# Performance work log

Measured on AMD Instinct MI355X. Metric: run time of the kernel, lower is better.

Reference implementation:

```python
import jax, jax.numpy as jnp
import numpy as np

B, N, E = 8192, 54, 144
F_NODE, F_EDGE, H, OUT = 18, 5, 48, 80
L = 3  # gnn_layers
LN_EPS = 1e-5


def mish(x):
    return x * jnp.tanh(jax.nn.softplus(x))


def setup_inputs() -> dict:
    key = jax.random.key(0)
    ks = jax.random.split(key, 24)
    s = 0.05
    inp = {
        "node_features": jax.random.normal(ks[0], (B, N, F_NODE), jnp.float32),
        "edge_features": jax.random.normal(ks[1], (B, E, F_EDGE), jnp.float32),
        # input projections
        "w_node": jax.random.normal(ks[2], (F_NODE, H), jnp.float32) * s,
        "b_node": jnp.zeros((H,), jnp.float32),
        "w_edge": jax.random.normal(ks[3], (F_EDGE, H), jnp.float32) * s,
        "b_edge": jnp.zeros((H,), jnp.float32),
        # stacked per-layer params (leading dim = L)
        "msg_w1": jax.random.normal(ks[4], (L, 3 * H, H), jnp.float32) * s,
        "msg_b1": jnp.zeros((L, H), jnp.float32),
        "msg_w2": jax.random.normal(ks[5], (L, H, H), jnp.float32) * s,
        "msg_b2": jnp.zeros((L, H), jnp.float32),
        "upd_w1": jax.random.normal(ks[6], (L, 2 * H, H), jnp.float32) * s,
        "upd_b1": jnp.zeros((L, H), jnp.float32),
        "upd_w2": jax.random.normal(ks[7], (L, H, H), jnp.float32) * s,
        "upd_b2": jnp.zeros((L, H), jnp.float32),
        "ln_g": jnp.ones((L, H), jnp.float32),
        "ln_b": jnp.zeros((L, H), jnp.float32),
        # output projection
        "w_out1": jax.random.normal(ks[8], (2 * H, OUT), jnp.float32) * s,
        "b_out1": jnp.zeros((OUT,), jnp.float32),
        "w_out2": jax.random.normal(ks[9], (OUT, OUT), jnp.float32) * s,
        "b_out2": jnp.zeros((OUT,), jnp.float32),
        "edge_index": jax.random.randint(ks[10], (2, E), 0, N, jnp.int64)
        if jax.config.jax_enable_x64 else jax.random.randint(ks[10], (2, E), 0, N, jnp.int32),
    }
    return inp


def reference(node_features, edge_features, w_node, b_node, w_edge, b_edge,
              msg_w1, msg_b1, msg_w2, msg_b2,
              upd_w1, upd_b1, upd_w2, upd_b2, ln_g, ln_b,
              w_out1, b_out1, w_out2, b_out2, edge_index):
    Bv, Nv, _ = node_features.shape
    Ev = edge_features.shape[1]
    h = mish(node_features @ w_node + b_node)            # [B,N,H]
    e = edge_features @ w_edge + b_edge                  # [B,E,H]
    h_flat = h.reshape(Bv * Nv, H)
    e_flat = e.reshape(Bv * Ev, H)
    offsets = jnp.arange(Bv, dtype=edge_index.dtype) * Nv
    src = (edge_index[0][None, :] + offsets[:, None]).reshape(-1)  # [B*E]
    dst = (edge_index[1][None, :] + offsets[:, None]).reshape(-1)
    for l in range(L):
        m = jnp.concatenate([h_flat[src], h_flat[dst], e_flat], axis=-1)  # [B*E,3H]
        m = mish(m @ msg_w1[l] + msg_b1[l])
        m = mish(m @ msg_w2[l] + msg_b2[l])
        agg = jax.ops.segment_sum(m, dst, num_segments=Bv * Nv)  # scatter-add
        u = jnp.concatenate([h_flat, agg], axis=-1)              # [B*N,2H]
        u = mish(u @ upd_w1[l] + upd_b1[l])
        u = u @ upd_w2[l] + upd_b2[l]
        x = h_flat + u
        mu = jnp.mean(x, axis=-1, keepdims=True)
        var = jnp.mean((x - mu) ** 2, axis=-1, keepdims=True)
        h_flat = (x - mu) * jax.lax.rsqrt(var + LN_EPS) * ln_g[l] + ln_b[l]
    node_emb = h_flat.reshape(Bv, Nv, H)
    mean_pool = node_emb.mean(axis=1)
    max_pool = node_emb.max(axis=1)
    pooled = jnp.concatenate([mean_pool, max_pool], axis=-1)     # [B,2H]
    board_emb = mish(pooled @ w_out1 + b_out1) @ w_out2 + b_out2  # [B,OUT]
    return board_emb, node_emb
```

## Files before the change

kernel.cpp:

```cpp
#include <hip/hip_runtime.h>

#define NGR 8192
#define NN 54
#define NE 144
#define FN 18
#define FE 5
#define HD 48
#define NOUT 80
#define NL 3
#define HS 56
#define MS 72
#define TS 152
#define NFRAG 102

typedef short v8s __attribute__((ext_vector_type(8)));
typedef float v4f __attribute__((ext_vector_type(4)));

#define MFMA(a, b, c) __builtin_amdgcn_mfma_f32_16x16x32_bf16((a), (b), (c), 0, 0, 0)

static __device__ __forceinline__ float mish_f(float x) {
  float t = __expf(x);
  float s = 1.0f + t;
  float s2 = s * s;
  float r = (s2 - 1.0f) * __builtin_amdgcn_rcpf(s2 + 1.0f);
  return (x > 20.0f) ? x : x * r;
}
static __device__ __forceinline__ short f2b(float x) {
  union { float f; unsigned u; } v; v.f = x;
  unsigned r = v.u + 0x7FFFu + ((v.u >> 16) & 1u);
  return (short)(r >> 16);
}
static __device__ __forceinline__ float b2f(short s) {
  union { unsigned u; float f; } v; v.u = ((unsigned)(unsigned short)s) << 16;
  return v.f;
}
static __device__ __forceinline__ unsigned pk2(float a, float b) {
  return (unsigned)(unsigned short)f2b(a) | ((unsigned)(unsigned short)f2b(b) << 16);
}

__global__ void gnn_setup(const float* __restrict__ w_node,
                          const float* __restrict__ w_edge,
                          const float* __restrict__ b_edge,
                          const float* __restrict__ msg_w1,
                          const float* __restrict__ msg_b1,
                          const float* __restrict__ msg_w2,
                          const float* __restrict__ upd_w1,
                          const float* __restrict__ upd_w2,
                          float* __restrict__ mb1, short* __restrict__ frags) {
  const int t = threadIdx.x;
  if (blockIdx.x == 0) {
    for (int idx = t; idx < NL * HD; idx += 256) {
      int l = idx / HD, c = idx % HD;
      float s = msg_b1[l * HD + c];
      for (int k = 0; k < HD; ++k)
        s += b_edge[k] * msg_w1[(l * 144 + 96 + k) * HD + c];
      mb1[idx] = s;
    }
  }
  for (int eid = blockIdx.x * 256 + t; eid < NFRAG * 512; eid += gridDim.x * 256) {
    int f = eid >> 9, r = eid & 511;
    int lane = r >> 3, j = r & 7;
    int kk = ((lane >> 4) << 3) + j;
    int colq = lane & 15;
    float val = 0.f;
    if (f < 3) {
      int c = f * 16 + colq;
      if (kk < FN) val = w_node[kk * HD + c];
    } else {
      int g = f - 3, l = g / 33, o = g % 33;
      if (o < 9) {
        int ks = o / 3, ct = o % 3, c = ct * 16 + colq, k = ks * 32 + kk;
        val = msg_w1[(l * 144 + k) * HD + c];
      } else if (o < 12) {
        int ct = o - 9, c = ct * 16 + colq;
        if (kk < FE) {
          float s = 0.f;
          for (int k2 = 0; k2 < HD; ++k2)
            s += w_edge[kk * HD + k2] * msg_w1[(l * 144 + 96 + k2) * HD + c];
          val = s;
        }
      } else if (o < 18) {
        int oo = o - 12, ks = oo / 3, ct = oo % 3, c = ct * 16 + colq, k = ks * 32 + kk;
        if (k < HD) val = msg_w2[(l * HD + k) * HD + c];
      } else if (o < 27) {
        int oo = o - 18, ks = oo / 3, ct = oo % 3, c = ct * 16 + colq, k = ks * 32 + kk;
        val = upd_w1[(l * 96 + k) * HD + c];
      } else {
        int oo = o - 27, ks = oo / 3, ct = oo % 3, c = ct * 16 + colq, k = ks * 32 + kk;
        if (k < HD) val = upd_w2[(l * HD + k) * HD + c];
      }
    }
    frags[eid] = f2b(val);
  }
}

__global__ __launch_bounds__(256, 4) void gnn_main(
    const float* __restrict__ nf, const float* __restrict__ efx,
    const float* __restrict__ b_node,
    const float* __restrict__ msg_b2,
    const float* __restrict__ upd_b1, const float* __restrict__ upd_b2,
    const float* __restrict__ ln_g, const float* __restrict__ ln_b,
    const float* __restrict__ w_out1, const float* __restrict__ b_out1,
    const float* __restrict__ w_out2, const float* __restrict__ b_out2,
    const int* __restrict__ edge_index,
    const float* __restrict__ mb1, const short* __restrict__ frags,
    float* __restrict__ out)
{
  __shared__ __align__(16) short h_s[NN][HS];
  __shared__ __align__(16) short agg_s[NN][HS];
  __shared__ __align__(16) short m_s[80][MS];
  __shared__ __align__(16) short m_t[48 * TS + 8];
  __shared__ int dst_s[NE];
  __shared__ float psum[96], pmax[96], pooled[96], o1[NOUT];

  const int b = blockIdx.x;
  const int t = threadIdx.x;
  const int lane = t & 63;
  const int w = t >> 6;
  const int lx = lane & 15;
  const int lg = lane >> 4;
  const int koff = lg << 3;
  const int lg4 = lg << 2;

#define LD8(f) (*(const v8s*)(frags + ((size_t)(f) << 9) + (lane << 3)))

  if (t < NE) dst_s[t] = edge_index[NE + t];
  for (int idx = t; idx < 64 * 32; idx += 256) {
    int r = idx >> 5, c = idx & 31;
    m_s[r][c] = (r < NN && c < FN) ? f2b(nf[(size_t)b * (NN * FN) + r * FN + c]) : (short)0;
  }
  for (int idx = t; idx < 80 * 16; idx += 256)
    m_s[idx >> 4][48 + (idx & 15)] = 0;
  for (int idx = t; idx < 48 * 8; idx += 256)
    m_t[(idx >> 3) * TS + 144 + (idx & 7)] = 0;
  if (t < 8) m_t[48 * TS + t] = 0;

  const int mt0 = w, mt2 = 5 + w;
  int rs0 = edge_index[mt0 * 16 + lx] * HS, rd0 = edge_index[NE + mt0 * 16 + lx] * HS;
  int rs1 = 0, rd1 = 0;
  if (w == 0) { rs1 = edge_index[64 + lx] * HS; rd1 = edge_index[NE + 64 + lx] * HS; }
  int rs2 = edge_index[mt2 * 16 + lx] * HS, rd2 = edge_index[NE + mt2 * 16 + lx] * HS;

  auto ldef = [&](int mt) -> v8s {
    v8s r = {0, 0, 0, 0, 0, 0, 0, 0};
    if (lg == 0) {
      const float* ep = efx + (size_t)b * (NE * FE) + (mt * 16 + lx) * FE;
      r[0] = f2b(ep[0]); r[1] = f2b(ep[1]); r[2] = f2b(ep[2]);
      r[3] = f2b(ep[3]); r[4] = f2b(ep[4]);
    }
    return r;
  };
  v8s aef0 = ldef(mt0);
  v8s aef1 = (w == 0) ? ldef(4) : (v8s){0,0,0,0,0,0,0,0};
  v8s aef2 = ldef(mt2);

  __syncthreads();

  const short* h0 = &h_s[0][0];
  const short* g0 = &agg_s[0][0];

  {
    v8s a = *(const v8s*)(&m_s[w * 16 + lx][koff]);
    const int orow = w * 16 + lg4;
    #pragma unroll
    for (int nt = 0; nt < 3; ++nt) {
      float bb = b_node[nt * 16 + lx];
      v4f c = {bb, bb, bb, bb};
      c = MFMA(a, LD8(nt), c);
      #pragma unroll
      for (int r = 0; r < 4; ++r)
        if (orow + r < NN) h_s[orow + r][nt * 16 + lx] = f2b(mish_f(c[r]));
    }
  }
  __syncthreads();

  for (int l = 0; l < NL; ++l) {
    const int FB = 3 + l * 33;
    float bm1[3], bm2[3];
    #pragma unroll
    for (int nt = 0; nt < 3; ++nt) {
      bm1[nt] = mb1[l * HD + nt * 16 + lx];
      bm2[nt] = msg_b2[(size_t)l * HD + nt * 16 + lx];
    }

    auto do_msg = [&](int mt, int slot, v8s aef, int rs, int rd) {
      v4f c0 = {bm1[0], bm1[0], bm1[0], bm1[0]};
      v4f c1 = {bm1[1], bm1[1], bm1[1], bm1[1]};
      v4f c2 = {bm1[2], bm1[2], bm1[2], bm1[2]};
      c0 = MFMA(aef, LD8(FB + 9),  c0);
      c1 = MFMA(aef, LD8(FB + 10), c1);
      c2 = MFMA(aef, LD8(FB + 11), c2);
      #pragma unroll
      for (int ks = 0; ks < 3; ++ks) {
        int kk = ks * 32 + koff;
        const short* p = (kk < HD) ? (h0 + rs + kk) : (h0 + rd + (kk - HD));
        v8s a = *(const v8s*)p;
        c0 = MFMA(a, LD8(FB + ks * 3 + 0), c0);
        c1 = MFMA(a, LD8(FB + ks * 3 + 1), c1);
        c2 = MFMA(a, LD8(FB + ks * 3 + 2), c2);
      }
      const int orow = slot + lg4;
      #pragma unroll
      for (int r = 0; r < 4; ++r) {
        m_s[orow + r][lx]      = f2b(mish_f(c0[r]));
        m_s[orow + r][16 + lx] = f2b(mish_f(c1[r]));
        m_s[orow + r][32 + lx] = f2b(mish_f(c2[r]));
      }
      v8s a0 = *(const v8s*)(&m_s[slot + lx][koff]);
      v8s a1 = *(const v8s*)(&m_s[slot + lx][32 + koff]);
      #pragma unroll
      for (int nt = 0; nt < 3; ++nt) {
        v4f c = {bm2[nt], bm2[nt], bm2[nt], bm2[nt]};
        c = MFMA(a0, LD8(FB + 12 + nt), c);
        c = MFMA(a1, LD8(FB + 15 + nt), c);
        uint2 u;
        u.x = pk2(mish_f(c[0]), mish_f(c[1]));
        u.y = pk2(mish_f(c[2]), mish_f(c[3]));
        *(uint2*)(&m_t[(nt * 16 + lx) * TS + mt * 16 + lg4]) = u;
      }
    };
    do_msg(mt0, w * 16, aef0, rs0, rd0);
    if (w == 0) do_msg(4, 64, aef1, rs1, rd1);
    do_msg(mt2, w * 16, aef2, rs2, rd2);
    __syncthreads();

    const int node = w * 16 + lx;
    {
      v8s sfr[5];
      #pragma unroll
      for (int kt = 0; kt < 5; ++kt) {
        v8s sv = {0, 0, 0, 0, 0, 0, 0, 0};
        #pragma unroll
        for (int j = 0; j < 8; ++j) {
          int e = kt * 32 + koff + j;
          if (e < NE && dst_s[e] == node) sv[j] = (short)0x3F80;
        }
        sfr[kt] = sv;
      }
      #pragma unroll
      for (int ct = 0; ct < 3; ++ct) {
        v4f c = {0.f, 0.f, 0.f, 0.f};
        #pragma unroll
        for (int kt = 0; kt < 5; ++kt) {
          v8s a = *(const v8s*)(&m_t[(ct * 16 + lx) * TS + kt * 32 + koff]);
          c = MFMA(a, sfr[kt], c);
        }
        if (node < NN) {
          uint2 u; u.x = pk2(c[0], c[1]); u.y = pk2(c[2], c[3]);
          *(uint2*)(&agg_s[node][ct * 16 + lg4]) = u;
        }
      }
    }
    {
      const int nrd = (node < NN) ? node : 0;
      v4f c0 = {upd_b1[l*HD + lx],      upd_b1[l*HD + lx],      upd_b1[l*HD + lx],      upd_b1[l*HD + lx]};
      v4f c1 = {upd_b1[l*HD + 16 + lx], upd_b1[l*HD + 16 + lx], upd_b1[l*HD + 16 + lx], upd_b1[l*HD + 16 + lx]};
      v4f c2 = {upd_b1[l*HD + 32 + lx], upd_b1[l*HD + 32 + lx], upd_b1[l*HD + 32 + lx], upd_b1[l*HD + 32 + lx]};
      #pragma unroll
      for (int ks = 0; ks < 3; ++ks) {
        int kk = ks * 32 + koff;
        const short* p = (kk < HD) ? (h0 + nrd * HS + kk) : (g0 + nrd * HS + (kk - HD));
        v8s a = *(const v8s*)p;
        c0 = MFMA(a, LD8(FB + 18 + ks * 3 + 0), c0);
        c1 = MFMA(a, LD8(FB + 18 + ks * 3 + 1), c1);
        c2 = MFMA(a, LD8(FB + 18 + ks * 3 + 2), c2);
      }
      const int orow = w * 16 + lg4;
      #pragma unroll
      for (int r = 0; r < 4; ++r) {
        m_s[orow + r][lx]      = f2b(mish_f(c0[r]));
        m_s[orow + r][16 + lx] = f2b(mish_f(c1[r]));
        m_s[orow + r][32 + lx] = f2b(mish_f(c2[r]));
      }
      v8s a0 = *(const v8s*)(&m_s[node][koff]);
      v8s a1 = *(const v8s*)(&m_s[node][32 + koff]);
      v4f cc[3];
      #pragma unroll
      for (int nt = 0; nt < 3; ++nt) {
        float bb = upd_b2[(size_t)l * HD + nt * 16 + lx];
        v4f c = {bb, bb, bb, bb};
        c = MFMA(a0, LD8(FB + 27 + nt), c);
        c = MFMA(a1, LD8(FB + 30 + nt), c);
        cc[nt] = c;
      }
      float x[3][4], s[4], q[4];
      #pragma unroll
      for (int r = 0; r < 4; ++r) {
        int rr = (orow + r < NN) ? (orow + r) : 0;
        #pragma unroll
        for (int nt = 0; nt < 3; ++nt)
          x[nt][r] = cc[nt][r] + b2f(h_s[rr][nt * 16 + lx]);
        s[r] = x[0][r] + x[1][r] + x[2][r];
        q[r] = fmaf(x[0][r], x[0][r], fmaf(x[1][r], x[1][r], x[2][r] * x[2][r]));
      }
      #pragma unroll
      for (int mask = 1; mask <= 8; mask <<= 1)
        #pragma unroll
        for (int r = 0; r < 4; ++r) {
          s[r] += __shfl_xor(s[r], mask);
          q[r] += __shfl_xor(q[r], mask);
        }
      float* onode = out + (size_t)NGR * NOUT + (size_t)b * (NN * HD);
      #pragma unroll
      for (int r = 0; r < 4; ++r) {
        float mu = s[r] * (1.f / HD);
        float var = q[r] * (1.f / HD) - mu * mu;
        float rsg = rsqrtf(var + 1e-5f);
        int row = orow + r;
        #pragma unroll
        for (int nt = 0; nt < 3; ++nt) {
          float y = (x[nt][r] - mu) * rsg * ln_g[l * HD + nt * 16 + lx] + ln_b[l * HD + nt * 16 + lx];
          if (row < NN) {
            h_s[row][nt * 16 + lx] = f2b(y);
            if (l == NL - 1) onode[row * HD + nt * 16 + lx] = y;
          }
        }
      }
    }
    __syncthreads();
  }

  if (t < 96) {
    int half = t >= HD;
    int ch = t - half * HD;
    float smv = 0.f, mx = -3.0e38f;
    int n0 = half * 27;
    for (int n = n0; n < n0 + 27; ++n) {
      float v = b2f(h_s[n][ch]);
      smv += v; mx = fmaxf(mx, v);
    }
    psum[t] = smv; pmax[t] = mx;
  }
  __syncthreads();
  if (t < HD) {
    pooled[t] = (psum[t] + psum[HD + t]) * (1.f / NN);
    pooled[HD + t] = fmaxf(pmax[t], pmax[HD + t]);
  }
  __syncthreads();

  if (t < NOUT) {
    float a = b_out1[t];
    #pragma unroll 8
    for (int k = 0; k < 2 * HD; ++k) a = fmaf(pooled[k], w_out1[k * NOUT + t], a);
    o1[t] = mish_f(a);
  }
  __syncthreads();
  if (t < NOUT) {
    float a = b_out2[t];
    #pragma unroll 8
    for (int k = 0; k < NOUT; ++k) a = fmaf(o1[k], w_out2[k * NOUT + t], a);
    out[(size_t)b * NOUT + t] = a;
  }
}

extern "C" void kernel_launch(void* const* d_in, const int* in_sizes, int n_in,
                              void* d_out, int out_size, void* d_ws, size_t ws_size,
                              hipStream_t stream) {
  const float* nf     = (const float*)d_in[0];
  const float* ef     = (const float*)d_in[1];
  const float* w_node = (const float*)d_in[2];
  const float* b_node = (const float*)d_in[3];
  const float* w_edge = (const float*)d_in[4];
  const float* b_edge = (const float*)d_in[5];
  const float* msg_w1 = (const float*)d_in[6];
  const float* msg_b1 = (const float*)d_in[7];
  const float* msg_w2 = (const float*)d_in[8];
  const float* msg_b2 = (const float*)d_in[9];
  const float* upd_w1 = (const float*)d_in[10];
  const float* upd_b1 = (const float*)d_in[11];
  const float* upd_w2 = (const float*)d_in[12];
  const float* upd_b2 = (const float*)d_in[13];
  const float* ln_g   = (const float*)d_in[14];
  const float* ln_b   = (const float*)d_in[15];
  const float* w_out1 = (const float*)d_in[16];
  const float* b_out1 = (const float*)d_in[17];
  const float* w_out2 = (const float*)d_in[18];
  const float* b_out2 = (const float*)d_in[19];
  const int* edge_index = (const int*)d_in[20];

  float* mb1   = (float*)d_ws;
  short* frags = (short*)((char*)d_ws + 1024);

  gnn_setup<<<32, 256, 0, stream>>>(w_node, w_edge, b_edge, msg_w1, msg_b1,
                                    msg_w2, upd_w1, upd_w2, mb1, frags);
  gnn_main<<<NGR, 256, 0, stream>>>(nf, ef, b_node, msg_b2, upd_b1, upd_b2,
                                    ln_g, ln_b, w_out1, b_out1, w_out2, b_out2,
                                    edge_index, mb1, frags, (float*)d_out);
}
```

Baseline: 483.5 us.

## Transpose MFMA operands so each lane owns a row, hoist weight fragments, use hw bf16 pack

Swaps the MFMA A/B operand order so accumulators come out transposed: each lane holds 4 consecutive channels of one row. Mish outputs and LayerNorm results can then be written as packed 8-byte stores, and the LayerNorm reduction needs 2 cross-lane shuffles instead of 4 per row-register. Message-layer weight fragments are hoisted into registers once per layer, and bias, gamma and beta are loaded as float4 vectors. Mish is simplified to an algebraically equivalent form with a clamp, and bf16 packing uses the hardware v_cvt_pk_bf16_f32 instruction; the extra register pressure may lower occupancy.

```diff
diff --git a/kernel.cpp b/kernel.cpp
--- a/kernel.cpp
+++ b/kernel.cpp
@@ -19,11 +19,9 @@
 #define MFMA(a, b, c) __builtin_amdgcn_mfma_f32_16x16x32_bf16((a), (b), (c), 0, 0, 0)
 
 static __device__ __forceinline__ float mish_f(float x) {
-  float t = __expf(x);
-  float s = 1.0f + t;
-  float s2 = s * s;
-  float r = (s2 - 1.0f) * __builtin_amdgcn_rcpf(s2 + 1.0f);
-  return (x > 20.0f) ? x : x * r;
+  float t = __expf(fminf(x, 30.f));
+  float u = t * (t + 2.f);
+  return x * u * __builtin_amdgcn_rcpf(u + 2.f);
 }
 static __device__ __forceinline__ short f2b(float x) {
   union { float f; unsigned u; } v; v.f = x;
@@ -34,8 +32,18 @@
   union { unsigned u; float f; } v; v.u = ((unsigned)(unsigned short)s) << 16;
   return v.f;
 }
-static __device__ __forceinline__ unsigned pk2(float a, float b) {
-  return (unsigned)(unsigned short)f2b(a) | ((unsigned)(unsigned short)f2b(b) << 16);
+static __device__ __forceinline__ unsigned cvt_pk(float lo, float hi) {
+  unsigned r;
+  asm("v_cvt_pk_bf16_f32 %0, %1, %2" : "=v"(r) : "v"(lo), "v"(hi));
+  return r;
+}
+static __device__ __forceinline__ void st4v(short* p, v4f y) {
+  uint2 u; u.x = cvt_pk(y[0], y[1]); u.y = cvt_pk(y[2], y[3]);
+  *(uint2*)p = u;
+}
+static __device__ __forceinline__ void st4m(short* p, v4f c) {
+  v4f y; y[0] = mish_f(c[0]); y[1] = mish_f(c[1]); y[2] = mish_f(c[2]); y[3] = mish_f(c[3]);
+  st4v(p, y);
 }
 
 __global__ void gnn_setup(const float* __restrict__ w_node,
@@ -157,65 +165,67 @@
   __syncthreads();
 
   const short* h0 = &h_s[0][0];
-  const short* g0 = &agg_s[0][0];
+  const int node = w * 16 + lx;
+  const int nrd = (node < NN) ? node : 0;
 
   {
-    v8s a = *(const v8s*)(&m_s[w * 16 + lx][koff]);
-    const int orow = w * 16 + lg4;
-    #pragma unroll
-    for (int nt = 0; nt < 3; ++nt) {
-      float bb = b_node[nt * 16 + lx];
-      v4f c = {bb, bb, bb, bb};
-      c = MFMA(a, LD8(nt), c);
-      #pragma unroll
-      for (int r = 0; r < 4; ++r)
-        if (orow + r < NN) h_s[orow + r][nt * 16 + lx] = f2b(mish_f(c[r]));
+    v8s a = *(const v8s*)(&m_s[node][koff]);
+    #pragma unroll
+    for (int ct = 0; ct < 3; ++ct) {
+      v4f c = *(const v4f*)(b_node + ct * 16 + lg4);
+      c = MFMA(LD8(ct), a, c);
+      if (node < NN) st4m(&h_s[node][ct * 16 + lg4], c);
     }
   }
   __syncthreads();
 
   for (int l = 0; l < NL; ++l) {
     const int FB = 3 + l * 33;
-    float bm1[3], bm2[3];
-    #pragma unroll
-    for (int nt = 0; nt < 3; ++nt) {
-      bm1[nt] = mb1[l * HD + nt * 16 + lx];
-      bm2[nt] = msg_b2[(size_t)l * HD + nt * 16 + lx];
-    }
+    v8s bw1[3][3], bwe[3], bw2[2][3];
+    #pragma unroll
+    for (int ks = 0; ks < 3; ++ks)
+      #pragma unroll
+      for (int ct = 0; ct < 3; ++ct) bw1[ks][ct] = LD8(FB + ks * 3 + ct);
+    #pragma unroll
+    for (int ct = 0; ct < 3; ++ct) bwe[ct] = LD8(FB + 9 + ct);
+    #pragma unroll
+    for (int ks = 0; ks < 2; ++ks)
+      #pragma unroll
+      for (int ct = 0; ct < 3; ++ct) bw2[ks][ct] = LD8(FB + 12 + ks * 3 + ct);
+    float bm2[3];
+    #pragma unroll
+    for (int nt = 0; nt < 3; ++nt) bm2[nt] = msg_b2[(size_t)l * HD + nt * 16 + lx];
 
     auto do_msg = [&](int mt, int slot, v8s aef, int rs, int rd) {
-      v4f c0 = {bm1[0], bm1[0], bm1[0], bm1[0]};
-      v4f c1 = {bm1[1], bm1[1], bm1[1], bm1[1]};
-      v4f c2 = {bm1[2], bm1[2], bm1[2], bm1[2]};
-      c0 = MFMA(aef, LD8(FB + 9),  c0);
-      c1 = MFMA(aef, LD8(FB + 10), c1);
-      c2 = MFMA(aef, LD8(FB + 11), c2);
+      v4f c0 = *(const v4f*)(mb1 + l * HD + lg4);
+      v4f c1 = *(const v4f*)(mb1 + l * HD + 16 + lg4);
+      v4f c2 = *(const v4f*)(mb1 + l * HD + 32 + lg4);
+      c0 = MFMA(bwe[0], aef, c0);
+      c1 = MFMA(bwe[1], aef, c1);
+      c2 = MFMA(bwe[2], aef, c2);
       #pragma unroll
       for (int ks = 0; ks < 3; ++ks) {
         int kk = ks * 32 + koff;
         const short* p = (kk < HD) ? (h0 + rs + kk) : (h0 + rd + (kk - HD));
         v8s a = *(const v8s*)p;
-        c0 = MFMA(a, LD8(FB + ks * 3 + 0), c0);
-        c1 = MFMA(a, LD8(FB + ks * 3 + 1), c1);
-        c2 = MFMA(a, LD8(FB + ks * 3 + 2), c2);
-      }
-      const int orow = slot + lg4;
-      #pragma unroll
-      for (int r = 0; r < 4; ++r) {
-        m_s[orow + r][lx]      = f2b(mish_f(c0[r]));
-        m_s[orow + r][16 + lx] = f2b(mish_f(c1[r]));
-        m_s[orow + r][32 + lx] = f2b(mish_f(c2[r]));
-      }
-      v8s a0 = *(const v8s*)(&m_s[slot + lx][koff]);
-      v8s a1 = *(const v8s*)(&m_s[slot + lx][32 + koff]);
+        c0 = MFMA(bw1[ks][0], a, c0);
+        c1 = MFMA(bw1[ks][1], a, c1);
+        c2 = MFMA(bw1[ks][2], a, c2);
+      }
+      short* mr = &m_s[slot + lx][0];
+      st4m(mr + lg4, c0);
+      st4m(mr + 16 + lg4, c1);
+      st4m(mr + 32 + lg4, c2);
+      v8s a0 = *(const v8s*)(mr + koff);
+      v8s a1 = *(const v8s*)(mr + 32 + koff);
       #pragma unroll
       for (int nt = 0; nt < 3; ++nt) {
         v4f c = {bm2[nt], bm2[nt], bm2[nt], bm2[nt]};
-        c = MFMA(a0, LD8(FB + 12 + nt), c);
-        c = MFMA(a1, LD8(FB + 15 + nt), c);
+        c = MFMA(a0, bw2[0][nt], c);
+        c = MFMA(a1, bw2[1][nt], c);
         uint2 u;
-        u.x = pk2(mish_f(c[0]), mish_f(c[1]));
-        u.y = pk2(mish_f(c[2]), mish_f(c[3]));
+        u.x = cvt_pk(mish_f(c[0]), mish_f(c[1]));
+        u.y = cvt_pk(mish_f(c[2]), mish_f(c[3]));
         *(uint2*)(&m_t[(nt * 16 + lx) * TS + mt * 16 + lg4]) = u;
       }
     };
@@ -224,7 +234,6 @@
     do_msg(mt2, w * 16, aef2, rs2, rd2);
     __syncthreads();
 
-    const int node = w * 16 + lx;
     {
       v8s sfr[5];
       #pragma unroll
@@ -245,75 +254,64 @@
           v8s a = *(const v8s*)(&m_t[(ct * 16 + lx) * TS + kt * 32 + koff]);
           c = MFMA(a, sfr[kt], c);
         }
-        if (node < NN) {
-          uint2 u; u.x = pk2(c[0], c[1]); u.y = pk2(c[2], c[3]);
-          *(uint2*)(&agg_s[node][ct * 16 + lg4]) = u;
-        }
+        if (node < NN) st4v(&agg_s[node][ct * 16 + lg4], c);
       }
     }
     {
-      const int nrd = (node < NN) ? node : 0;
-      v4f c0 = {upd_b1[l*HD + lx],      upd_b1[l*HD + lx],      upd_b1[l*HD + lx],      upd_b1[l*HD + lx]};
-      v4f c1 = {upd_b1[l*HD + 16 + lx], upd_b1[l*HD + 16 + lx], upd_b1[l*HD + 16 + lx], upd_b1[l*HD + 16 + lx]};
-      v4f c2 = {upd_b1[l*HD + 32 + lx], upd_b1[l*HD + 32 + lx], upd_b1[l*HD + 32 + lx], upd_b1[l*HD + 32 + lx]};
+      v4f c0 = *(const v4f*)(upd_b1 + l * HD + lg4);
+      v4f c1 = *(const v4f*)(upd_b1 + l * HD + 16 + lg4);
+      v4f c2 = *(const v4f*)(upd_b1 + l * HD + 32 + lg4);
       #pragma unroll
       for (int ks = 0; ks < 3; ++ks) {
         int kk = ks * 32 + koff;
-        const short* p = (kk < HD) ? (h0 + nrd * HS + kk) : (g0 + nrd * HS + (kk - HD));
+        const short* p = (kk < HD) ? (&h_s[nrd][kk]) : (&agg_s[nrd][kk - HD]);
         v8s a = *(const v8s*)p;
-        c0 = MFMA(a, LD8(FB + 18 + ks * 3 + 0), c0);
-        c1 = MFMA(a, LD8(FB + 18 + ks * 3 + 1), c1);
-        c2 = MFMA(a, LD8(FB + 18 + ks * 3 + 2), c2);
-      }
-      const int orow = w * 16 + lg4;
-      #pragma unroll
-      for (int r = 0; r < 4; ++r) {
-        m_s[orow + r][lx]      = f2b(mish_f(c0[r]));
-        m_s[orow + r][16 + lx] = f2b(mish_f(c1[r]));
-        m_s[orow + r][32 + lx] = f2b(mish_f(c2[r]));
-      }
-      v8s a0 = *(const v8s*)(&m_s[node][koff]);
-      v8s a1 = *(const v8s*)(&m_s[node][32 + koff]);
+        c0 = MFMA(LD8(FB + 18 + ks * 3 + 0), a, c0);
+        c1 = MFMA(LD8(FB + 18 + ks * 3 + 1), a, c1);
+        c2 = MFMA(LD8(FB + 18 + ks * 3 + 2), a, c2);
+      }
+      short* ur = &m_s[node][0];
+      st4m(ur + lg4, c0);
+      st4m(ur + 16 + lg4, c1);
+      st4m(ur + 32 + lg4, c2);
+      v8s a0 = *(const v8s*)(ur + koff);
+      v8s a1 = *(const v8s*)(ur + 32 + koff);
       v4f cc[3];
       #pragma unroll
-      for (int nt = 0; nt < 3; ++nt) {
-        float bb = upd_b2[(size_t)l * HD + nt * 16 + lx];
-        v4f c = {bb, bb, bb, bb};
-        c = MFMA(a0, LD8(FB + 27 + nt), c);
-        c = MFMA(a1, LD8(FB + 30 + nt), c);
-        cc[nt] = c;
-      }
-      float x[3][4], s[4], q[4];
-      #pragma unroll
-      for (int r = 0; r < 4; ++r) {
-        int rr = (orow + r < NN) ? (orow + r) : 0;
+      for (int ct = 0; ct < 3; ++ct) {
+        v4f c = *(const v4f*)(upd_b2 + l * HD + ct * 16 + lg4);
+        c = MFMA(LD8(FB + 27 + ct), a0, c);
+        c = MFMA(LD8(FB + 30 + ct), a1, c);
+        cc[ct] = c;
+      }
+      float x[3][4];
+      float s = 0.f, q = 0.f;
+      #pragma unroll
+      for (int ct = 0; ct < 3; ++ct) {
+        uint2 hv = *(const uint2*)(&h_s[nrd][ct * 16 + lg4]);
+        x[ct][0] = cc[ct][0] + __uint_as_float(hv.x << 16);
+        x[ct][1] = cc[ct][1] + __uint_as_float(hv.x & 0xFFFF0000u);
+        x[ct][2] = cc[ct][2] + __uint_as_float(hv.y << 16);
+        x[ct][3] = cc[ct][3] + __uint_as_float(hv.y & 0xFFFF0000u);
         #pragma unroll
-        for (int nt = 0; nt < 3; ++nt)
-          x[nt][r] = cc[nt][r] + b2f(h_s[rr][nt * 16 + lx]);
-        s[r] = x[0][r] + x[1][r] + x[2][r];
-        q[r] = fmaf(x[0][r], x[0][r], fmaf(x[1][r], x[1][r], x[2][r] * x[2][r]));
-      }
-      #pragma unroll
-      for (int mask = 1; mask <= 8; mask <<= 1)
+        for (int r = 0; r < 4; ++r) { s += x[ct][r]; q = fmaf(x[ct][r], x[ct][r], q); }
+      }
+      s += __shfl_xor(s, 16); s += __shfl_xor(s, 32);
+      q += __shfl_xor(q, 16); q += __shfl_xor(q, 32);
+      float mu = s * (1.f / HD);
+      float var = q * (1.f / HD) - mu * mu;
+      float rsg = rsqrtf(var + 1e-5f);
+      float* onode = out + (size_t)NGR * NOUT + (size_t)b * (NN * HD);
+      #pragma unroll
+      for (int ct = 0; ct < 3; ++ct) {
+        v4f g4 = *(const v4f*)(ln_g + l * HD + ct * 16 + lg4);
+        v4f b4 = *(const v4f*)(ln_b + l * HD + ct * 16 + lg4);
+        v4f y;
         #pragma unroll
-        for (int r = 0; r < 4; ++r) {
-          s[r] += __shfl_xor(s[r], mask);
-          q[r] += __shfl_xor(q[r], mask);
-        }
-      float* onode = out + (size_t)NGR * NOUT + (size_t)b * (NN * HD);
-      #pragma unroll
-      for (int r = 0; r < 4; ++r) {
-        float mu = s[r] * (1.f / HD);
-        float var = q[r] * (1.f / HD) - mu * mu;
-        float rsg = rsqrtf(var + 1e-5f);
-        int row = orow + r;
-        #pragma unroll
-        for (int nt = 0; nt < 3; ++nt) {
-          float y = (x[nt][r] - mu) * rsg * ln_g[l * HD + nt * 16 + lx] + ln_b[l * HD + nt * 16 + lx];
-          if (row < NN) {
-            h_s[row][nt * 16 + lx] = f2b(y);
-            if (l == NL - 1) onode[row * HD + nt * 16 + lx] = y;
-          }
+        for (int r = 0; r < 4; ++r) y[r] = (x[ct][r] - mu) * rsg * g4[r] + b4[r];
+        if (node < NN) {
+          st4v(&h_s[node][ct * 16 + lg4], y);
+          if (l == NL - 1) *(v4f*)(onode + node * HD + ct * 16 + lg4) = y;
         }
       }
     }
```

Measured after the change: 547.8 us. 1.13x slower.
